# Kernel optimization log

Hardware: AMD Instinct MI355X
Metric: run time of the kernel (lower is better)

The kernel has to match this reference:

```python
import jax, jax.numpy as jnp
import numpy as np
import math

B, C, H, W = 2, 256, 64, 64
E = 256           # embed_dim
AE = 64           # angle embed dim = embed_dim // 4
NH = 3            # num angle hypotheses
HEADS = 8
HALF = AE // 2    # 32 sin/cos frequencies

# 3x3 kernel tap grid (dy, dx), row-major, matching torchvision DeformConv2d tap order
KY = jnp.array([-1,-1,-1, 0,0,0, 1,1,1], jnp.float32)
KX = jnp.array([-1, 0, 1,-1,0,1,-1,0,1], jnp.float32)
# assumed angle hypothesis deltas around the predicted angle
HYPO_DELTAS = (-math.pi/12, 0.0, math.pi/12)


def conv2d(x, w, b, pad):
    y = jax.lax.conv_general_dilated(x, w, (1, 1), [(pad, pad), (pad, pad)],
                                     dimension_numbers=('NCHW', 'OIHW', 'NCHW'))
    return y + b[None, :, None, None]


def gen_offsets(angles):
    """Rotate the base 3x3 kernel taps by the per-pixel angle; offset = rotated - base.
    angles: (B, H*W, 1) -> offsets (B, 18, H, W), (dy,dx) interleaved per tap."""
    a = angles.reshape(-1, H, W)
    c = jnp.cos(a)[..., None]           # (B,H,W,1)
    s = jnp.sin(a)[..., None]
    ry = KX * s + KY * c                # rotated y of each tap, (B,H,W,9)
    rx = KX * c - KY * s                # rotated x
    off = jnp.stack([ry - KY, rx - KX], axis=-1)   # (B,H,W,9,2)
    return off.reshape(-1, H, W, 18).transpose(0, 3, 1, 2)


def deform_conv(x, offsets, w, b):
    """DeformConv2d k=3, stride=1, pad=1, dilation=1, zero padding outside.
    x (B,C,H,W), offsets (B,18,H,W), w (O,C,3,3)."""
    off = offsets.reshape(x.shape[0], 9, 2, H, W)
    oy = off[:, :, 0].transpose(0, 2, 3, 1)          # (B,H,W,9)
    ox = off[:, :, 1].transpose(0, 2, 3, 1)
    hh = jnp.arange(H, dtype=jnp.float32)[None, :, None, None]
    ww = jnp.arange(W, dtype=jnp.float32)[None, None, :, None]
    py = hh + KY + oy                                # sample y, (B,H,W,9)
    px = ww + KX + ox
    y0 = jnp.floor(py)
    x0 = jnp.floor(px)
    wy = (py - y0)[:, None]                          # (B,1,H,W,9)
    wx = (px - x0)[:, None]

    def gather(yi, xi):
        valid = (yi >= 0) & (yi <= H - 1) & (xi >= 0) & (xi <= W - 1)
        yc = jnp.clip(yi, 0, H - 1).astype(jnp.int32)
        xc = jnp.clip(xi, 0, W - 1).astype(jnp.int32)
        g = jax.vmap(lambda img, yy, xx: img[:, yy, xx])(x, yc, xc)  # (B,C,H,W,9)
        return g * valid[:, None].astype(x.dtype)

    samp = (gather(y0, x0) * (1 - wy) * (1 - wx)
            + gather(y0, x0 + 1) * (1 - wy) * wx
            + gather(y0 + 1, x0) * wy * (1 - wx)
            + gather(y0 + 1, x0 + 1) * wy * wx)      # (B,C,H,W,9)
    w9 = w.reshape(w.shape[0], w.shape[1], 9)
    return jnp.einsum('bchwk,ock->bohw', samp, w9) + b[None, :, None, None]


def angle_encode(angles, freq_mult, w1, b1, ln_g, ln_b, w2, b2):
    an = (angles / (math.pi / 2))[..., 0]                       # (B,HW) le90 norm
    dim_t = jnp.arange(HALF, dtype=jnp.float32) / HALF * math.pi
    ae = an[..., None] * (freq_mult * dim_t)                    # (B,HW,HALF)
    emb = jnp.concatenate([jnp.sin(ae), jnp.cos(ae)], axis=-1)  # (B,HW,AE)
    h = emb @ w1.T + b1
    mu = h.mean(-1, keepdims=True)
    var = h.var(-1, keepdims=True)
    h = (h - mu) * jax.lax.rsqrt(var + 1e-5) * ln_g + ln_b
    return jax.nn.relu(h) @ w2.T + b2


def mha(q, kv, in_w, in_b, out_w, out_b):
    # q (L,1,E), kv (L,NH,E); torch nn.MultiheadAttention math
    wq, wk, wv = jnp.split(in_w, 3, axis=0)
    bq, bk, bv = jnp.split(in_b, 3)
    hd = E // HEADS
    Q = (q @ wq.T + bq).reshape(-1, 1, HEADS, hd).transpose(0, 2, 1, 3)
    K = (kv @ wk.T + bk).reshape(-1, NH, HEADS, hd).transpose(0, 2, 1, 3)
    V = (kv @ wv.T + bv).reshape(-1, NH, HEADS, hd).transpose(0, 2, 1, 3)
    attn = jax.nn.softmax(jnp.einsum('lhqd,lhkd->lhqk', Q, K) / math.sqrt(hd), axis=-1)
    o = jnp.einsum('lhqk,lhkd->lhqd', attn, V).transpose(0, 2, 1, 3).reshape(-1, 1, E)
    return o @ out_w.T + out_b


def group_norm(x, g, b, groups=32, eps=1e-5):
    Bq, Cc, Hh, Ww = x.shape
    xg = x.reshape(Bq, groups, Cc // groups, Hh, Ww)
    mu = xg.mean((2, 3, 4), keepdims=True)
    var = xg.var((2, 3, 4), keepdims=True)
    xn = ((xg - mu) * jax.lax.rsqrt(var + eps)).reshape(x.shape)
    return xn * g[None, :, None, None] + b[None, :, None, None]


def setup_inputs() -> dict:
    key = jax.random.key(0)
    ks = iter(jax.random.split(key, 32))
    r = lambda *s: jax.random.normal(next(ks), s, jnp.float32) * 0.05
    z = lambda *s: jnp.zeros(s, jnp.float32)
    return {
        'features': jax.random.normal(next(ks), (B, C, H, W), jnp.float32),
        'ap_w1': r(C // 4, C, 3, 3), 'ap_b1': z(C // 4),
        'ap_w2': r(1, C // 4, 1, 1), 'ap_b2': z(1),
        'freq_mult': jnp.ones((HALF,), jnp.float32),
        'ae_w1': r(AE, AE), 'ae_b1': z(AE),
        'ae_ln_g': jnp.ones((AE,), jnp.float32), 'ae_ln_b': z(AE),
        'ae_w2': r(AE, AE), 'ae_b2': z(AE),
        'dc_w': r(E, C, 3, 3), 'dc_b': z(E),
        'attn_in_w': r(3 * E, E), 'attn_in_b': z(3 * E),
        'attn_out_w': r(E, E), 'attn_out_b': z(E),
        'ja_w1': r(E, E + AE, 1, 1), 'ja_b1': z(E),
        'ja_w2': r(E, E, 1, 1), 'ja_b2': z(E),
        'op_w1': r(E, E, 3, 3), 'op_b1': z(E),
        'gn_g': jnp.ones((E,), jnp.float32), 'gn_b': z(E),
        'op_w2': r(E, E, 1, 1), 'op_b2': z(E),
    }


def reference(features, ap_w1, ap_b1, ap_w2, ap_b2, freq_mult, ae_w1, ae_b1,
              ae_ln_g, ae_ln_b, ae_w2, ae_b2, dc_w, dc_b, attn_in_w, attn_in_b,
              attn_out_w, attn_out_b, ja_w1, ja_b1, ja_w2, ja_b2, op_w1, op_b1,
              gn_g, gn_b, op_w2, op_b2):
    # 1) angle prediction
    h1 = jax.nn.relu(conv2d(features, ap_w1, ap_b1, 1))
    angles = conv2d(h1, ap_w2, ap_b2, 0).reshape(B, H * W, 1)
    # 2) periodic angle encoding
    angle_embed = angle_encode(angles, freq_mult, ae_w1, ae_b1, ae_ln_g, ae_ln_b, ae_w2, ae_b2)
    # 3) rotation-aware deformable alignment
    aligned = deform_conv(features, gen_offsets(angles), dc_w, dc_b)
    # 4) multi-angle hypotheses fused by per-pixel attention
    cand = [deform_conv(features, gen_offsets(angles + d), dc_w, dc_b) for d in HYPO_DELTAS]
    feat_stack = jnp.stack(cand, axis=1)                       # (B,NH,E,H,W)
    q = aligned.transpose(0, 2, 3, 1).reshape(B * H * W, 1, E)
    kv = feat_stack.transpose(0, 3, 4, 1, 2).reshape(B * H * W, NH, E)
    fused = mha(q, kv, attn_in_w, attn_in_b, attn_out_w, attn_out_b)
    fused = fused.reshape(B, H, W, E).transpose(0, 3, 1, 2)
    # 5) joint angle-spatial attention gate
    ae_sp = angle_embed.reshape(B, H, W, AE).transpose(0, 3, 1, 2)
    ji = jnp.concatenate([fused, ae_sp], axis=1)
    gate = jax.nn.sigmoid(conv2d(jax.nn.relu(conv2d(ji, ja_w1, ja_b1, 0)), ja_w2, ja_b2, 0))
    enh = fused * gate + fused
    # 6) output projection
    o = jax.nn.relu(group_norm(conv2d(enh, op_w1, op_b1, 1), gn_g, gn_b))
    return conv2d(o, op_w2, op_b2, 0)
```

## Files before the change

kernel.cpp:

```cpp
#include <hip/hip_runtime.h>

#define PI_F 3.14159265358979323846f
#define HWSZ 4096
#define NPIX 8192

typedef __attribute__((ext_vector_type(8))) short short8;
typedef __attribute__((ext_vector_type(4))) short short4_t;
typedef __attribute__((ext_vector_type(4))) float f32x4;

__device__ __forceinline__ short f2bf(float x){
  unsigned u = __float_as_uint(x);
  unsigned r = (u + 0x7FFFu + ((u >> 16) & 1u)) >> 16;
  return (short)r;
}
__device__ __forceinline__ float bf2f(short v){
  return __uint_as_float(((unsigned)(unsigned short)v) << 16);
}

__device__ __forceinline__ float wsum64(float v){
  #pragma unroll
  for (int m = 32; m >= 1; m >>= 1) v += __shfl_xor(v, m, 64);
  return v;
}
__device__ __forceinline__ float wsum8(float v){
  v += __shfl_xor(v, 1, 64);
  v += __shfl_xor(v, 2, 64);
  v += __shfl_xor(v, 4, 64);
  return v;
}

__device__ __forceinline__ void gl_lds(const short* g, short* s){
  __builtin_amdgcn_global_load_lds(
      (const __attribute__((address_space(1))) unsigned int*)g,
      (__attribute__((address_space(3))) unsigned int*)s, 16, 0, 0);
}

__global__ void k_prepall(const float* __restrict__ dc_w, const float* __restrict__ op_w1,
    const float* __restrict__ ap_w1, const float* __restrict__ features,
    const float* __restrict__ s0, const float* __restrict__ s1,
    const float* __restrict__ s2, const float* __restrict__ s3, const float* __restrict__ s4,
    short* __restrict__ enh_pad, short* __restrict__ Bdc, short* __restrict__ B2op,
    short* __restrict__ B3, short* __restrict__ feat_bf, short* __restrict__ A3,
    short* __restrict__ d0, short* __restrict__ d1,
    short* __restrict__ d2, short* __restrict__ d3, short* __restrict__ d4){
  __shared__ short tile[2304];
  __shared__ float ft[32][33];
  int bx = blockIdx.x, tid = threadIdx.x;
  if (bx < 2178){
    int i = bx*256 + tid;
    if (i < 557568) ((short4_t*)enh_pad)[i] = (short4_t){0,0,0,0};
  } else if (bx < 2434){
    int o = bx - 2178;
    const float* wo = dc_w + (size_t)o*2304;
    for (int i = tid; i < 2304; i += 256){
      int c = i / 9, k = i - c*9;
      tile[k*256 + c] = f2bf(wo[i]);
    }
    __syncthreads();
    for (int i = tid; i < 2304; i += 256){
      int k = i >> 8, c = i & 255;
      Bdc[((size_t)(k*256 + o))*256 + c] = tile[i];
    }
  } else if (bx < 2690){
    int o = bx - 2434;
    const float* wo = op_w1 + (size_t)o*2304;
    for (int i = tid; i < 2304; i += 256){
      int c = i / 9, k = i - c*9;
      tile[k*256 + c] = f2bf(wo[i]);
    }
    __syncthreads();
    short* out = B2op + (size_t)o*2304;
    for (int i = tid; i < 2304; i += 256) out[i] = tile[i];
  } else if (bx < 3330){
    int n = bx - 2690, c = tid;
    short hi = 0;
    if (n < 576){
      int o = n & 63, k = n >> 6;
      hi = f2bf(ap_w1[((size_t)o*256 + c)*9 + k]);
    }
    B3[(size_t)n*512 + c] = hi;
    B3[(size_t)n*512 + 256 + c] = hi;
  } else if (bx < 5186){
    int i = (bx - 3330)*256 + tid;
    if (i < 196608) d0[i] = f2bf(s0[i]);
    else if (i < 262144) d1[i-196608] = f2bf(s1[i-196608]);
    else if (i < 344064) d2[i-262144] = f2bf(s2[i-262144]);
    else if (i < 409600) d3[i-344064] = f2bf(s3[i-344064]);
    else if (i < 475136) d4[i-409600] = f2bf(s4[i-409600]);
  } else {
    int bid = bx - 5186;
    int z = bid >> 10;
    int rem = bid & 1023;
    int p0 = (rem & 127)*32, c0 = (rem >> 7)*32;
    int tx = tid & 31, ty = tid >> 5;
    #pragma unroll
    for (int i = ty; i < 32; i += 8)
      ft[i][tx] = features[((size_t)z*256 + c0 + i)*HWSZ + p0 + tx];
    __syncthreads();
    #pragma unroll
    for (int i = ty; i < 32; i += 8){
      float x = ft[tx][i];
      short hi = f2bf(x);
      short lo = f2bf(x - bf2f(hi));
      size_t p = (size_t)z*HWSZ + p0 + i;
      feat_bf[p*256 + c0 + tx] = hi;
      A3[p*512 + c0 + tx] = hi;
      A3[p*512 + 256 + c0 + tx] = lo;
    }
  }
}

template<int EPI, int BM, int BN = 128>
__global__ __launch_bounds__(256) void k_gemml(const short* __restrict__ A,
    const short* __restrict__ B, void* __restrict__ Cv,
    const float* __restrict__ bias, const short* __restrict__ aux,
    int K, int ldc){
  constexpr int NWC = BN/64;
  constexpr int NWR = 4/NWC;
  constexpr int WM = BM/NWR;
  constexpr int AF = WM/16;
  __shared__ alignas(16) short sA[2][BM*32];
  __shared__ alignas(16) short sB[2][BN*32];
  int tid = threadIdx.x;
  int w = tid >> 6, l = tid & 63;
  int wc = w % NWC, wr = w / NWC;
  int ml = l & 15, g = l >> 4;
  int srow = tid >> 2;
  int sch = (tid & 3)*8;
  int m0 = blockIdx.x*BM, n0 = blockIdx.y*BN;
  const short* Agp = A + (size_t)(m0 + srow)*K + sch;
  const short* Bgp = B + (size_t)(n0 + srow)*K + sch;
  short* sAd = &sA[0][srow*32 + sch];
  short* sBd = &sB[0][srow*32 + sch];
  f32x4 acc[AF][4];
  #pragma unroll
  for (int i = 0; i < AF; ++i)
    #pragma unroll
    for (int j = 0; j < 4; ++j) acc[i][j] = (f32x4){0.f,0.f,0.f,0.f};

  #define STAGE(bf, kt) { \
    _Pragma("unroll") \
    for (int c = 0; c < BM/64; ++c) \
      gl_lds(Agp + (size_t)(c*64)*K + (kt)*32, sAd + (bf)*BM*32 + c*2048); \
    _Pragma("unroll") \
    for (int c = 0; c < BN/64; ++c) \
      gl_lds(Bgp + (size_t)(c*64)*K + (kt)*32, sBd + (bf)*BN*32 + c*2048); \
  }
  int nk = K >> 5;
  STAGE(0, 0)
  int buf = 0;
  for (int kt = 0; kt < nk; ++kt){
    __syncthreads();
    if (kt + 1 < nk){ STAGE(buf^1, kt+1) }
    short8 af[AF], bq[4];
    #pragma unroll
    for (int i = 0; i < AF; ++i)
      af[i] = *(const short8*)&sA[buf][(wr*WM + i*16 + ml)*32 + g*8];
    #pragma unroll
    for (int j = 0; j < 4; ++j)
      bq[j] = *(const short8*)&sB[buf][(wc*64 + j*16 + ml)*32 + g*8];
    #pragma unroll
    for (int i = 0; i < AF; ++i)
      #pragma unroll
      for (int j = 0; j < 4; ++j)
        acc[i][j] = __builtin_amdgcn_mfma_f32_16x16x32_bf16(af[i], bq[j], acc[i][j], 0, 0, 0);
    buf ^= 1;
  }
  #undef STAGE

  int m0w = m0 + wr*WM;
  int n0w = n0 + wc*64;
  if constexpr (EPI == 4){
    __shared__ float cst[BM][129];
    #pragma unroll
    for (int fm = 0; fm < AF; ++fm)
      #pragma unroll
      for (int fn = 0; fn < 4; ++fn)
        #pragma unroll
        for (int r = 0; r < 4; ++r){
          int cl = wc*64 + fn*16 + ml;
          cst[wr*WM + fm*16 + g*4 + r][cl] = acc[fm][fn][r] + bias[blockIdx.y*128 + cl];
        }
    __syncthreads();
    int px0 = blockIdx.x*BM;
    int b = px0 >> 12, hw0 = px0 & 4095;
    int o = tid >> 1, seg = (tid & 1)*(BM/2);
    float* op = (float*)Cv + (((size_t)(b*256 + blockIdx.y*128 + o)) << 12) + hw0 + seg;
    #pragma unroll
    for (int i = 0; i < BM/2; i += 4){
      float4 vv = {cst[seg+i][o], cst[seg+i+1][o], cst[seg+i+2][o], cst[seg+i+3][o]};
      *(float4*)(op + i) = vv;
    }
  } else {
    #pragma unroll
    for (int fm = 0; fm < AF; ++fm)
      #pragma unroll
      for (int fn = 0; fn < 4; ++fn)
        #pragma unroll
        for (int r = 0; r < 4; ++r){
          int row = m0w + fm*16 + g*4 + r;
          int col = n0w + fn*16 + ml;
          float v = acc[fm][fn][r];
          if constexpr (EPI == 0){
            ((short*)Cv)[(size_t)row*ldc + col] = f2bf(v);
          } else if constexpr (EPI == 1){
            ((short*)Cv)[(size_t)row*ldc + col] = f2bf(v + bias[col]);
          } else if constexpr (EPI == 2){
            ((short*)Cv)[(size_t)row*ldc + col] = f2bf(fmaxf(v + bias[col], 0.f));
          } else if constexpr (EPI == 3){
            float f = bf2f(aux[(size_t)row*320 + col]);
            float s = 1.f/(1.f + __expf(-(v + bias[col])));
            ((short*)Cv)[(size_t)row*ldc + col] = f2bf(f * (1.f + s));
          } else if constexpr (EPI == 6){
            float f = bf2f(aux[(size_t)row*320 + col]);
            float s = 1.f/(1.f + __expf(-(v + bias[col])));
            int b = row >> 12, hw = row & 4095;
            int pi = b*4356 + ((hw>>6)+1)*66 + (hw&63) + 1;
            ((short*)Cv)[(size_t)pi*256 + col] = f2bf(f * (1.f + s));
          } else if constexpr (EPI == 7){
            ((short*)Cv)[(size_t)(col>>8)*2097152 + (size_t)row*256 + (col&255)] = f2bf(v);
          } else {
            ((float*)Cv)[(size_t)row*ldc + col] = v;
          }
        }
  }
}

__global__ __launch_bounds__(256) void k_qkv(const short* __restrict__ cand,
    const short* __restrict__ inw, const float* __restrict__ inb,
    short* __restrict__ KV, short* __restrict__ Qb){
  const short* A; const short* B; short* C; const float* bias; int ldc, m0, n0;
  if (blockIdx.y < 4){
    A = cand; B = inw + (size_t)256*256; C = KV; bias = inb + 256; ldc = 512;
    m0 = blockIdx.x*128; n0 = blockIdx.y*128;
  } else {
    if (blockIdx.x >= 128) return;
    A = cand + (size_t)NPIX*256; B = inw; C = Qb; bias = inb; ldc = 256;
    m0 = (blockIdx.x >> 1)*128; n0 = (blockIdx.x & 1)*128;
  }
  __shared__ alignas(16) short sA[2][128*32];
  __shared__ alignas(16) short sB[2][128*32];
  int tid = threadIdx.x;
  int w = tid >> 6, l = tid & 63;
  int wc = w & 1, wr = w >> 1;
  int ml = l & 15, g = l >> 4;
  int srow = tid >> 2;
  int sch = (tid & 3)*8;
  const short* Agp = A + (size_t)(m0 + srow)*256 + sch;
  const short* Bgp = B + (size_t)(n0 + srow)*256 + sch;
  short* sAd = &sA[0][srow*32 + sch];
  short* sBd = &sB[0][srow*32 + sch];
  f32x4 acc[4][4];
  #pragma unroll
  for (int i = 0; i < 4; ++i)
    #pragma unroll
    for (int j = 0; j < 4; ++j) acc[i][j] = (f32x4){0.f,0.f,0.f,0.f};
  #define STG2(bf, kt) { \
    gl_lds(Agp + (kt)*32, sAd + (bf)*4096); \
    gl_lds(Agp + (size_t)64*256 + (kt)*32, sAd + (bf)*4096 + 2048); \
    gl_lds(Bgp + (kt)*32, sBd + (bf)*4096); \
    gl_lds(Bgp + (size_t)64*256 + (kt)*32, sBd + (bf)*4096 + 2048); \
  }
  STG2(0, 0)
  int buf = 0;
  for (int kt = 0; kt < 8; ++kt){
    __syncthreads();
    if (kt + 1 < 8){ STG2(buf^1, kt+1) }
    short8 af[4], bq[4];
    #pragma unroll
    for (int i = 0; i < 4; ++i)
      af[i] = *(const short8*)&sA[buf][(wr*64 + i*16 + ml)*32 + g*8];
    #pragma unroll
    for (int j = 0; j < 4; ++j)
      bq[j] = *(const short8*)&sB[buf][(wc*64 + j*16 + ml)*32 + g*8];
    #pragma unroll
    for (int i = 0; i < 4; ++i)
      #pragma unroll
      for (int j = 0; j < 4; ++j)
        acc[i][j] = __builtin_amdgcn_mfma_f32_16x16x32_bf16(af[i], bq[j], acc[i][j], 0, 0, 0);
    buf ^= 1;
  }
  #undef STG2
  int m0w = m0 + wr*64;
  int n0w = n0 + wc*64;
  #pragma unroll
  for (int fm = 0; fm < 4; ++fm)
    #pragma unroll
    for (int fn = 0; fn < 4; ++fn)
      #pragma unroll
      for (int r = 0; r < 4; ++r){
        int row = m0w + fm*16 + g*4 + r;
        int col = n0w + fn*16 + ml;
        C[(size_t)row*ldc + col] = f2bf(acc[fm][fn][r] + bias[col]);
      }
}

__global__ __launch_bounds__(256) void k_attnproj(const short* __restrict__ Qb,
    const short* __restrict__ KVb, const short* __restrict__ wot,
    const float* __restrict__ outb, short* __restrict__ gateA){
  __shared__ alignas(16) short sO[64*256];
  __shared__ alignas(16) short sB[2][64*32];
  int tid = threadIdx.x;
  int m0 = blockIdx.x*64, n0 = blockIdx.y*64;
  int srow = tid >> 2, sch = (tid & 3)*8;
  const short* Bgp = wot + (size_t)(n0 + srow)*256 + sch;
  short* sBd = &sB[0][srow*32 + sch];
  gl_lds(Bgp, sBd);
  int lane = tid & 63;
  int sub = tid >> 6;
  const float sc = 0.17677669529663688f;
  #pragma unroll 2
  for (int it = 0; it < 16; ++it){
    int lp = it*4 + sub;
    int p = m0 + lp;
    float q[4];
    { short4_t t = *(const short4_t*)(Qb + (size_t)p*256 + lane*4);
      #pragma unroll
      for (int j = 0; j < 4; ++j) q[j] = bf2f(t[j]); }
    float kv[3][2][4];
    #pragma unroll
    for (int i = 0; i < 3; ++i){
      const short* rp = KVb + (size_t)(i*NPIX + p)*512 + lane*4;
      short4_t kt = *(const short4_t*)rp;
      short4_t vt = *(const short4_t*)(rp + 256);
      #pragma unroll
      for (int j = 0; j < 4; ++j){ kv[i][0][j] = bf2f(kt[j]); kv[i][1][j] = bf2f(vt[j]); }
    }
    float s[3];
    #pragma unroll
    for (int i = 0; i < 3; ++i){
      float d = 0.f;
      #pragma unroll
      for (int j = 0; j < 4; ++j) d = fmaf(q[j], kv[i][0][j], d);
      s[i] = wsum8(d) * sc;
    }
    float m = fmaxf(s[0], fmaxf(s[1], s[2]));
    float e0 = __expf(s[0]-m), e1 = __expf(s[1]-m), e2 = __expf(s[2]-m);
    float inv = 1.f/(e0+e1+e2);
    short4_t ot;
    #pragma unroll
    for (int j = 0; j < 4; ++j)
      ot[j] = f2bf((e0*kv[0][1][j] + e1*kv[1][1][j] + e2*kv[2][1][j]) * inv);
    *(short4_t*)&sO[lp*256 + lane*4] = ot;
  }
  int w = sub, ml = lane & 15, g = lane >> 4;
  f32x4 acc[4];
  #pragma unroll
  for (int j = 0; j < 4; ++j) acc[j] = (f32x4){0.f,0.f,0.f,0.f};
  int buf = 0;
  for (int kt = 0; kt < 8; ++kt){
    __syncthreads();
    if (kt + 1 < 8) gl_lds(Bgp + (kt+1)*32, sBd + (buf^1)*2048);
    short8 af = *(const short8*)&sO[(w*16 + ml)*256 + kt*32 + g*8];
    short8 bq[4];
    #pragma unroll
    for (int j = 0; j < 4; ++j)
      bq[j] = *(const short8*)&sB[buf][(j*16 + ml)*32 + g*8];
    #pragma unroll
    for (int j = 0; j < 4; ++j)
      acc[j] = __builtin_amdgcn_mfma_f32_16x16x32_bf16(af, bq[j], acc[j], 0, 0, 0);
    buf ^= 1;
  }
  int m0w = m0 + w*16;
  #pragma unroll
  for (int fn = 0; fn < 4; ++fn)
    #pragma unroll
    for (int r = 0; r < 4; ++r){
      int row = m0w + g*4 + r;
      int col = n0 + fn*16 + ml;
      gateA[(size_t)row*320 + col] = f2bf(acc[fn][r] + outb[col]);
    }
}

__global__ __launch_bounds__(256) void k_igconv(const short* __restrict__ Xpad,
    const short* __restrict__ B2, float* __restrict__ PG){
  __shared__ alignas(16) short sA[2][64*32];
  __shared__ alignas(16) short sB[2][128*32];
  int zg = blockIdx.z;
  int tid = threadIdx.x;
  int w = tid >> 6, l = tid & 63;
  int wr = w & 1, wc = w >> 1;
  int ml = l & 15, g = l >> 4;
  int srow = tid >> 2;
  int sch = (tid & 3)*8;
  int m0 = blockIdx.x*64, n0 = blockIdx.y*128;
  int b = blockIdx.x >> 6, imgrow = blockIdx.x & 63;
  int qbase = b*4356 + (imgrow+1)*66 + srow + 1;
  const short* Bgp = B2 + (size_t)(n0 + srow)*2304 + zg*768 + sch;
  short* sAd = &sA[0][srow*32 + sch];
  short* sBd = &sB[0][srow*32 + sch];
  int toff[3];
  #pragma unroll
  for (int i = 0; i < 3; ++i){
    int t = zg*3 + i;
    toff[i] = (t/3 - 1)*66 + (t%3) - 1;
  }
  f32x4 acc[2][4];
  #pragma unroll
  for (int i = 0; i < 2; ++i)
    #pragma unroll
    for (int j = 0; j < 4; ++j) acc[i][j] = (f32x4){0.f,0.f,0.f,0.f};

  #define STG(bf, kt) { \
    int tap = (kt) >> 3, cofs = ((kt) & 7)*32; \
    gl_lds(Xpad + (size_t)(qbase + toff[tap])*256 + cofs + sch, sAd + (bf)*2048); \
    gl_lds(Bgp + (kt)*32, sBd + (bf)*4096); \
    gl_lds(Bgp + (size_t)64*2304 + (kt)*32, sBd + (bf)*4096 + 2048); \
  }
  STG(0, 0)
  int buf = 0;
  for (int kt = 0; kt < 24; ++kt){
    __syncthreads();
    if (kt < 23){ STG(buf^1, kt+1) }
    short8 af[2], bq[4];
    #pragma unroll
    for (int i = 0; i < 2; ++i)
      af[i] = *(const short8*)&sA[buf][(wr*32 + i*16 + ml)*32 + g*8];
    #pragma unroll
    for (int j = 0; j < 4; ++j)
      bq[j] = *(const short8*)&sB[buf][(wc*64 + j*16 + ml)*32 + g*8];
    #pragma unroll
    for (int i = 0; i < 2; ++i)
      #pragma unroll
      for (int j = 0; j < 4; ++j)
        acc[i][j] = __builtin_amdgcn_mfma_f32_16x16x32_bf16(af[i], bq[j], acc[i][j], 0, 0, 0);
    buf ^= 1;
  }
  #undef STG

  float* out = PG + (size_t)zg*2097152;
  int m0w = m0 + wr*32;
  int n0w = n0 + wc*64;
  #pragma unroll
  for (int fm = 0; fm < 2; ++fm)
    #pragma unroll
    for (int fn = 0; fn < 4; ++fn)
      #pragma unroll
      for (int r = 0; r < 4; ++r){
        int row = m0w + fm*16 + g*4 + r;
        int col = n0w + fn*16 + ml;
        out[(size_t)row*256 + col] = acc[fm][fn][r];
      }
}

__global__ void k_aph1enc(const float* __restrict__ T, const float* __restrict__ b1,
    const float* __restrict__ w2, const float* __restrict__ b2,
    const float* __restrict__ freq,
    const float* __restrict__ ew1, const float* __restrict__ eb1,
    const float* __restrict__ lng, const float* __restrict__ lnb,
    const float* __restrict__ ew2, const float* __restrict__ eb2,
    short* __restrict__ gateA, int2* __restrict__ moff, float4* __restrict__ mw){
  const int KYi[9] = {-1,-1,-1,0,0,0,1,1,1};
  const int KXi[9] = {-1,0,1,-1,0,1,-1,0,1};
  __shared__ float sang[4];
  int lane = threadIdx.x & 63;
  int wid = threadIdx.x >> 6;
  int p = blockIdx.x*4 + wid;
  int hw = p & 4095;
  int h = hw >> 6, w = hw & 63;
  float acc = b1[lane];
  #pragma unroll
  for (int k = 0; k < 9; ++k){
    int y = h + KYi[k], x = w + KXi[k];
    if (y < 0 || y > 63 || x < 0 || x > 63) continue;
    acc += T[(size_t)(p + KYi[k]*64 + KXi[k])*640 + k*64 + lane];
  }
  float av = wsum64(fmaxf(acc, 0.f) * w2[lane]) + b2[0];
  if (lane == 0) sang[wid] = av;
  float an = av * (2.0f / PI_F);
  int f = lane & 31;
  float ph = an * freq[f] * ((float)f * (PI_F / 32.0f));
  float emb = (lane < 32) ? __sinf(ph) : __cosf(ph);
  float hh = eb1[lane];
  const float* w1r = ew1 + lane*64;
  #pragma unroll 8
  for (int i = 0; i < 64; ++i){
    float e = __shfl(emb, i, 64);
    hh = fmaf(e, w1r[i], hh);
  }
  float mu = wsum64(hh) * (1.0f/64.0f);
  float d = hh - mu;
  float var = wsum64(d*d) * (1.0f/64.0f);
  float hn = fmaf(d * rsqrtf(var + 1e-5f), lng[lane], lnb[lane]);
  float r = fmaxf(hn, 0.f);
  float o = eb2[lane];
  const float* w2r = ew2 + lane*64;
  #pragma unroll 8
  for (int i = 0; i < 64; ++i){
    float e = __shfl(r, i, 64);
    o = fmaf(e, w2r[i], o);
  }
  gateA[(size_t)p*320 + 256 + lane] = f2bf(o);
  __syncthreads();
  int tid = threadIdx.x;
  if (tid < 108){
    int lp = tid / 27;
    int j = tid - lp*27;
    int pp = blockIdx.x*4 + lp;
    int hyp = j / 9;
    int tap = j - hyp*9;
    float ky = (float)(tap/3 - 1), kx = (float)(tap - (tap/3)*3 - 1);
    float a = sang[lp] + ((float)hyp - 1.0f) * (PI_F / 12.0f);
    float sn = __sinf(a), cs = __cosf(a);
    int b2i = pp >> 12, hw2 = pp & 4095;
    float py = (float)(hw2 >> 6) + kx*sn + ky*cs;
    float px = (float)(hw2 & 63) + kx*cs - ky*sn;
    float y0f = floorf(py), x0f = floorf(px);
    float wy = py - y0f, wx = px - x0f;
    int y0 = (int)y0f, x0 = (int)x0f;
    bool vx0 = (unsigned)x0 < 64u, vx1 = (unsigned)(x0+1) < 64u;
    bool vy0 = (unsigned)y0 < 64u, vy1 = (unsigned)(y0+1) < 64u;
    int xb = vx0 ? x0 : (vx1 ? x0+1 : 0);
    float sx0 = vx0 ? 1.f-wx : (vx1 ? wx : 0.f);
    float sx1 = (vx0 && vx1) ? wx : 0.f;
    int ry0 = vy0 ? y0 : 0;
    int ry1 = vy1 ? y0+1 : 0;
    float vw0 = vy0 ? 1.f-wy : 0.f;
    float vw1 = vy1 ? wy : 0.f;
    int base = (b2i << 12);
    int mi = pp*27 + j;
    moff[mi] = make_int2(tap*4194304 + (base + ry0*64 + xb)*512,
                         tap*4194304 + (base + ry1*64 + xb)*512);
    mw[mi] = make_float4(vw0*sx0, vw0*sx1, vw1*sx0, vw1*sx1);
  }
}

__global__ __launch_bounds__(256, 4) void k_sample(const short* __restrict__ G,
    const int2* __restrict__ moff, const float4* __restrict__ mw,
    const float* __restrict__ bias, short* __restrict__ cand){
  __shared__ int2 smo[216];
  __shared__ float4 smw[216];
  int id = blockIdx.x;
  int sw = (id & 7)*128 + (id >> 3);
  int tid = threadIdx.x;
  int pbase = sw*8;
  if (tid < 216){
    smo[tid] = moff[pbase*27 + tid];
    smw[tid] = mw[pbase*27 + tid];
  }
  __syncthreads();
  int lp = (tid >> 6)*2 + ((tid >> 5) & 1);
  int p = pbase + lp;
  int c8 = (tid & 31)*8;
  float av[3][8];
  {
    float4 b0 = *(const float4*)(bias + c8);
    float4 b1 = *(const float4*)(bias + c8 + 4);
    #pragma unroll
    for (int h2 = 0; h2 < 3; ++h2){
      av[h2][0]=b0.x; av[h2][1]=b0.y; av[h2][2]=b0.z; av[h2][3]=b0.w;
      av[h2][4]=b1.x; av[h2][5]=b1.y; av[h2][6]=b1.z; av[h2][7]=b1.w;
    }
  }
  #pragma unroll
  for (int hyp = 0; hyp < 3; ++hyp){
    #pragma unroll 3
    for (int tap = 0; tap < 9; ++tap){
      int idx = lp*27 + hyp*9 + tap;
      int2 o = smo[idx];
      float4 wv = smw[idx];
      const short* r0 = (const short*)((const char*)G + o.x) + c8;
      const short* r1 = (const short*)((const char*)G + o.y) + c8;
      short8 v00 = *(const short8*)r0;
      short8 v01 = *(const short8*)(r0 + 256);
      short8 v10 = *(const short8*)r1;
      short8 v11 = *(const short8*)(r1 + 256);
      #pragma unroll
      for (int e = 0; e < 8; ++e){
        float s = wv.x*bf2f(v00[e]) + wv.y*bf2f(v01[e]);
        s += wv.z*bf2f(v10[e]) + wv.w*bf2f(v11[e]);
        av[hyp][e] += s;
      }
    }
  }
  #pragma unroll
  for (int hyp = 0; hyp < 3; ++hyp){
    short8 o;
    #pragma unroll
    for (int e = 0; e < 8; ++e) o[e] = f2bf(av[hyp][e]);
    *(short8*)(cand + ((size_t)hyp*NPIX + p)*256 + c8) = o;
  }
}

__global__ void k_sum3stat(const float* __restrict__ PG, const float* __restrict__ bias,
    float* __restrict__ t, float* __restrict__ spart){
  int p0 = blockIdx.x * 8;
  int c = threadIdx.x;
  float bb = bias[c];
  float s = 0.f, s2 = 0.f;
  #pragma unroll
  for (int pp = 0; pp < 8; ++pp){
    size_t idx = (size_t)(p0+pp)*256 + c;
    float v = PG[idx] + PG[idx + 2097152] + PG[idx + 4194304] + bb;
    t[idx] = v;
    s += v; s2 = fmaf(v, v, s2);
  }
  s  += __shfl_xor(s, 1, 64);  s  += __shfl_xor(s, 2, 64);  s  += __shfl_xor(s, 4, 64);
  s2 += __shfl_xor(s2, 1, 64); s2 += __shfl_xor(s2, 2, 64); s2 += __shfl_xor(s2, 4, 64);
  if ((c & 7) == 0){
    int b = p0 >> 12;
    int bg = b*32 + (c >> 3);
    int blk = blockIdx.x & 511;
    spart[(size_t)(bg*512 + blk)*2]     = s;
    spart[(size_t)(bg*512 + blk)*2 + 1] = s2;
  }
}

__global__ void k_gnfin(const float* __restrict__ spart, float* __restrict__ stat){
  int bg = blockIdx.x;
  const float* sp = spart + (size_t)bg*1024;
  float s = 0.f, s2 = 0.f;
  for (int i = threadIdx.x; i < 512; i += 256){
    s += sp[i*2]; s2 += sp[i*2+1];
  }
  s = wsum64(s); s2 = wsum64(s2);
  __shared__ float rs[4], rs2[4];
  int wid = threadIdx.x >> 6;
  if ((threadIdx.x & 63) == 0){ rs[wid] = s; rs2[wid] = s2; }
  __syncthreads();
  if (threadIdx.x == 0){
    float S = rs[0]+rs[1]+rs[2]+rs[3];
    float S2 = rs2[0]+rs2[1]+rs2[2]+rs2[3];
    float mean = S * (1.f/32768.f);
    float var = S2 * (1.f/32768.f) - mean*mean;
    stat[bg*2]   = mean;
    stat[bg*2+1] = rsqrtf(var + 1e-5f);
  }
}

__global__ __launch_bounds__(256) void k_gnproj(const float* __restrict__ t,
    const float* __restrict__ stat, const float* __restrict__ gng,
    const float* __restrict__ gnb, const short* __restrict__ w2,
    const float* __restrict__ b2, float* __restrict__ out){
  __shared__ float cst[64*132];
  __shared__ alignas(16) short sB[2][128*32];
  short* sA = (short*)cst;
  int tid = threadIdx.x;
  int m0 = blockIdx.x*64;
  int b = m0 >> 12;
  int srow = tid >> 2, sch = (tid & 3)*8;
  const short* Bgp = w2 + (size_t)(blockIdx.y*128 + srow)*256 + sch;
  short* sBd = &sB[0][srow*32 + sch];
  gl_lds(Bgp, sBd);
  gl_lds(Bgp + (size_t)64*256, sBd + 2048);
  #pragma unroll 4
  for (int it = 0; it < 16; ++it){
    int c = it*256 + tid;
    int row = c >> 6;
    int col = (c & 63)*4;
    int g4 = col >> 3;
    float mean = stat[(b*32+g4)*2], rstd = stat[(b*32+g4)*2+1];
    float4 v = *(const float4*)(t + (size_t)(m0+row)*256 + col);
    float4 gg = *(const float4*)(gng + col);
    float4 bbv = *(const float4*)(gnb + col);
    short4_t o;
    o[0] = f2bf(fmaxf((v.x - mean)*rstd*gg.x + bbv.x, 0.f));
    o[1] = f2bf(fmaxf((v.y - mean)*rstd*gg.y + bbv.y, 0.f));
    o[2] = f2bf(fmaxf((v.z - mean)*rstd*gg.z + bbv.z, 0.f));
    o[3] = f2bf(fmaxf((v.w - mean)*rstd*gg.w + bbv.w, 0.f));
    *(short4_t*)&sA[row*256 + col] = o;
  }
  int w = tid >> 6, l = tid & 63;
  int wr = w & 1, wc = w >> 1;
  int ml = l & 15, g = l >> 4;
  f32x4 acc[2][4];
  #pragma unroll
  for (int i = 0; i < 2; ++i)
    #pragma unroll
    for (int j = 0; j < 4; ++j) acc[i][j] = (f32x4){0.f,0.f,0.f,0.f};
  int buf = 0;
  for (int kt = 0; kt < 8; ++kt){
    __syncthreads();
    if (kt + 1 < 8){
      gl_lds(Bgp + (kt+1)*32, sBd + (buf^1)*4096);
      gl_lds(Bgp + (size_t)64*256 + (kt+1)*32, sBd + (buf^1)*4096 + 2048);
    }
    short8 af[2], bq[4];
    #pragma unroll
    for (int i = 0; i < 2; ++i)
      af[i] = *(const short8*)&sA[(wr*32 + i*16 + ml)*256 + kt*32 + g*8];
    #pragma unroll
    for (int j = 0; j < 4; ++j)
      bq[j] = *(const short8*)&sB[buf][(wc*64 + j*16 + ml)*32 + g*8];
    #pragma unroll
    for (int i = 0; i < 2; ++i)
      #pragma unroll
      for (int j = 0; j < 4; ++j)
        acc[i][j] = __builtin_amdgcn_mfma_f32_16x16x32_bf16(af[i], bq[j], acc[i][j], 0, 0, 0);
    buf ^= 1;
  }
  __syncthreads();
  #pragma unroll
  for (int fm = 0; fm < 2; ++fm)
    #pragma unroll
    for (int fn = 0; fn < 4; ++fn)
      #pragma unroll
      for (int r = 0; r < 4; ++r){
        int cl = wc*64 + fn*16 + ml;
        cst[(wr*32 + fm*16 + g*4 + r)*132 + cl] = acc[fm][fn][r] + b2[blockIdx.y*128 + cl];
      }
  __syncthreads();
  int hw0 = m0 & 4095;
  int o = tid >> 1, seg = (tid & 1)*32;
  float* op = out + (((size_t)(b*256 + blockIdx.y*128 + o)) << 12) + hw0 + seg;
  #pragma unroll
  for (int i = 0; i < 32; i += 4){
    float4 vv = {cst[(seg+i)*132+o], cst[(seg+i+1)*132+o],
                 cst[(seg+i+2)*132+o], cst[(seg+i+3)*132+o]};
    *(float4*)(op + i) = vv;
  }
}

extern "C" void kernel_launch(void* const* d_in, const int* in_sizes, int n_in,
                              void* d_out, int out_size, void* d_ws, size_t ws_size,
                              hipStream_t stream){
  (void)in_sizes; (void)n_in; (void)out_size; (void)ws_size;
  const float* features   = (const float*)d_in[0];
  const float* ap_w1      = (const float*)d_in[1];
  const float* ap_b1      = (const float*)d_in[2];
  const float* ap_w2      = (const float*)d_in[3];
  const float* ap_b2      = (const float*)d_in[4];
  const float* freq       = (const float*)d_in[5];
  const float* ae_w1      = (const float*)d_in[6];
  const float* ae_b1      = (const float*)d_in[7];
  const float* ae_ln_g    = (const float*)d_in[8];
  const float* ae_ln_b    = (const float*)d_in[9];
  const float* ae_w2      = (const float*)d_in[10];
  const float* ae_b2      = (const float*)d_in[11];
  const float* dc_w       = (const float*)d_in[12];
  const float* dc_b       = (const float*)d_in[13];
  const float* attn_in_w  = (const float*)d_in[14];
  const float* attn_in_b  = (const float*)d_in[15];
  const float* attn_out_w = (const float*)d_in[16];
  const float* attn_out_b = (const float*)d_in[17];
  const float* ja_w1      = (const float*)d_in[18];
  const float* ja_b1      = (const float*)d_in[19];
  const float* ja_w2      = (const float*)d_in[20];
  const float* ja_b2      = (const float*)d_in[21];
  const float* op_w1      = (const float*)d_in[22];
  const float* op_b1      = (const float*)d_in[23];
  const float* gn_g       = (const float*)d_in[24];
  const float* gn_b       = (const float*)d_in[25];
  const float* op_w2      = (const float*)d_in[26];
  const float* op_b2      = (const float*)d_in[27];

  char* base = (char*)d_ws;
  #define ALLOC(ty, name, elems) ty* name = (ty*)base; base += (size_t)(elems)*sizeof(ty);
  ALLOC(short, feat_bf, 8192*256)
  ALLOC(short, Bdc,     2304*256)
  ALLOC(short, B2op,    256*2304)
  ALLOC(short, B3ap,    640*512)
  ALLOC(short, inw_bf,  768*256)
  ALLOC(short, wot_bf,  256*256)
  ALLOC(short, jw1_bf,  256*320)
  ALLOC(short, jw2_bf,  256*256)
  ALLOC(short, wop2_bf, 256*256)
  ALLOC(short, Gbuf,    24576*768)
  ALLOC(short, gguard,  64)
  ALLOC(short, cand_bf, 3*8192*256)
  ALLOC(short, gateA,   8192*320)
  ALLOC(short, hid_bf,  8192*256)
  ALLOC(short, enh_pad, 2*4356*256)
  ALLOC(float, tbuf,    8192*256)
  ALLOC(float, gstat,   128)
  ALLOC(float, spart,   65536)
  ALLOC(int,   moffb,   2*NPIX*27)
  ALLOC(float, mwb,     4*NPIX*27)
  #undef ALLOC
  (void)gguard;
  short* A3 = cand_bf;
  float* T_ap = (float*)Gbuf;
  short* KVbuf = Gbuf;
  short* Qbuf  = Gbuf + (size_t)24576*512;
  float* PG    = (float*)Gbuf;
  int2*  moff  = (int2*)moffb;
  float4* mwv  = (float4*)mwb;

  k_prepall<<<7234, 256, 0, stream>>>(dc_w, op_w1, ap_w1, features,
      attn_in_w, attn_out_w, ja_w1, ja_w2, op_w2,
      enh_pad, Bdc, B2op, B3ap, feat_bf, A3,
      inw_bf, wot_bf, jw1_bf, jw2_bf, wop2_bf);

  k_gemml<5,64><<<dim3(128,5), 256, 0, stream>>>(A3, B3ap, T_ap, nullptr, nullptr, 512, 640);
  k_aph1enc<<<2048, 256, 0, stream>>>(T_ap, ap_b1, ap_w2, ap_b2, freq,
                                      ae_w1, ae_b1, ae_ln_g, ae_ln_b, ae_w2, ae_b2,
                                      gateA, moff, mwv);
  k_gemml<7,128><<<dim3(64,18), 256, 0, stream>>>(feat_bf, Bdc, Gbuf, nullptr, nullptr, 256, 2304);
  k_sample<<<1024, 256, 0, stream>>>(Gbuf, moff, mwv, dc_b, cand_bf);
  k_qkv<<<dim3(192,5), 256, 0, stream>>>(cand_bf, inw_bf, attn_in_b, KVbuf, Qbuf);
  k_attnproj<<<dim3(128,4), 256, 0, stream>>>(Qbuf, KVbuf, wot_bf, attn_out_b, gateA);
  k_gemml<2,64,64><<<dim3(128,4), 256, 0, stream>>>(gateA, jw1_bf, hid_bf, ja_b1, nullptr, 320, 256);
  k_gemml<6,64,64><<<dim3(128,4), 256, 0, stream>>>(hid_bf, jw2_bf, enh_pad, ja_b2, gateA, 256, 256);
  k_igconv<<<dim3(128,2,3), 256, 0, stream>>>(enh_pad, B2op, PG);
  k_sum3stat<<<1024, 256, 0, stream>>>(PG, op_b1, tbuf, spart);
  k_gnfin<<<64, 256, 0, stream>>>(spart, gstat);
  k_gnproj<<<dim3(128,2), 256, 0, stream>>>(tbuf, gstat, gn_g, gn_b, wop2_bf, op_b2,
                                            (float*)d_out);
}
```

Measured before the change: 193.5 us.

## Merge angle-predictor GEMM and deform-conv tap GEMM into one launch

Combines the angle-predictor GEMM (A3 x B3, K=512) and the deform-conv tap GEMM (features x Bdc, K=256) into a single kernel whose grid y index chooses which GEMM a block computes. The deform GEMM now reads the hi half of A3 with stride 512, so the separate feat_bf copy and its writes in the prep kernel are removed. A3 and T_ap get their own workspace buffers instead of aliasing cand_bf and Gbuf, which the fused launch needs. This saves one launch and fills the GPU better, at the cost of more workspace memory and uneven per-block work (K=256 versus K=512 blocks).

```diff
diff --git a/kernel.cpp b/kernel.cpp
--- a/kernel.cpp
+++ b/kernel.cpp
@@ -40,7 +40,7 @@
     const float* __restrict__ s0, const float* __restrict__ s1,
     const float* __restrict__ s2, const float* __restrict__ s3, const float* __restrict__ s4,
     short* __restrict__ enh_pad, short* __restrict__ Bdc, short* __restrict__ B2op,
-    short* __restrict__ B3, short* __restrict__ feat_bf, short* __restrict__ A3,
+    short* __restrict__ B3, short* __restrict__ A3,
     short* __restrict__ d0, short* __restrict__ d1,
     short* __restrict__ d2, short* __restrict__ d3, short* __restrict__ d4){
   __shared__ short tile[2304];
@@ -103,11 +103,80 @@
       short hi = f2bf(x);
       short lo = f2bf(x - bf2f(hi));
       size_t p = (size_t)z*HWSZ + p0 + i;
-      feat_bf[p*256 + c0 + tx] = hi;
       A3[p*512 + c0 + tx] = hi;
       A3[p*512 + 256 + c0 + tx] = lo;
     }
   }
+}
+
+__global__ __launch_bounds__(256) void k_mainA(const short* __restrict__ A3,
+    const short* __restrict__ Bdc, const short* __restrict__ B3,
+    short* __restrict__ G, float* __restrict__ T){
+  __shared__ alignas(16) short sA[2][128*32];
+  __shared__ alignas(16) short sB[2][128*32];
+  bool isG = blockIdx.y < 18;
+  const short* B; int K, ldb, n0;
+  if (isG){ B = Bdc; K = 256; ldb = 256; n0 = blockIdx.y*128; }
+  else    { B = B3;  K = 512; ldb = 512; n0 = ((int)blockIdx.y - 18)*128; }
+  int tid = threadIdx.x;
+  int w = tid >> 6, l = tid & 63;
+  int wc = w & 1, wr = w >> 1;
+  int ml = l & 15, g = l >> 4;
+  int srow = tid >> 2;
+  int sch = (tid & 3)*8;
+  int m0 = blockIdx.x*128;
+  const short* Agp = A3 + (size_t)(m0 + srow)*512 + sch;
+  const short* Bgp = B + (size_t)(n0 + srow)*ldb + sch;
+  short* sAd = &sA[0][srow*32 + sch];
+  short* sBd = &sB[0][srow*32 + sch];
+  f32x4 acc[4][4];
+  #pragma unroll
+  for (int i = 0; i < 4; ++i)
+    #pragma unroll
+    for (int j = 0; j < 4; ++j) acc[i][j] = (f32x4){0.f,0.f,0.f,0.f};
+  #define STG(bf, kt) { \
+    gl_lds(Agp + (kt)*32, sAd + (bf)*4096); \
+    gl_lds(Agp + (size_t)64*512 + (kt)*32, sAd + (bf)*4096 + 2048); \
+    gl_lds(Bgp + (kt)*32, sBd + (bf)*4096); \
+    gl_lds(Bgp + (size_t)64*ldb + (kt)*32, sBd + (bf)*4096 + 2048); \
+  }
+  int nk = K >> 5;
+  STG(0, 0)
+  int buf = 0;
+  for (int kt = 0; kt < nk; ++kt){
+    __syncthreads();
+    if (kt + 1 < nk){ STG(buf^1, kt+1) }
+    short8 af[4], bq[4];
+    #pragma unroll
+    for (int i = 0; i < 4; ++i)
+      af[i] = *(const short8*)&sA[buf][(wr*64 + i*16 + ml)*32 + g*8];
+    #pragma unroll
+    for (int j = 0; j < 4; ++j)
+      bq[j] = *(const short8*)&sB[buf][(wc*64 + j*16 + ml)*32 + g*8];
+    #pragma unroll
+    for (int i = 0; i < 4; ++i)
+      #pragma unroll
+      for (int j = 0; j < 4; ++j)
+        acc[i][j] = __builtin_amdgcn_mfma_f32_16x16x32_bf16(af[i], bq[j], acc[i][j], 0, 0, 0);
+    buf ^= 1;
+  }
+  #undef STG
+  int m0w = m0 + wr*64;
+  int n0w = n0 + wc*64;
+  #pragma unroll
+  for (int fm = 0; fm < 4; ++fm)
+    #pragma unroll
+    for (int fn = 0; fn < 4; ++fn)
+      #pragma unroll
+      for (int r = 0; r < 4; ++r){
+        int row = m0w + fm*16 + g*4 + r;
+        int col = n0w + fn*16 + ml;
+        float v = acc[fm][fn][r];
+        if (isG)
+          G[(size_t)(col>>8)*2097152 + (size_t)row*256 + (col&255)] = f2bf(v);
+        else
+          T[(size_t)row*640 + col] = v;
+      }
 }
 
 template<int EPI, int BM, int BN = 128>
@@ -170,60 +239,25 @@
 
   int m0w = m0 + wr*WM;
   int n0w = n0 + wc*64;
-  if constexpr (EPI == 4){
-    __shared__ float cst[BM][129];
-    #pragma unroll
-    for (int fm = 0; fm < AF; ++fm)
-      #pragma unroll
-      for (int fn = 0; fn < 4; ++fn)
-        #pragma unroll
-        for (int r = 0; r < 4; ++r){
-          int cl = wc*64 + fn*16 + ml;
-          cst[wr*WM + fm*16 + g*4 + r][cl] = acc[fm][fn][r] + bias[blockIdx.y*128 + cl];
+  #pragma unroll
+  for (int fm = 0; fm < AF; ++fm)
+    #pragma unroll
+    for (int fn = 0; fn < 4; ++fn)
+      #pragma unroll
+      for (int r = 0; r < 4; ++r){
+        int row = m0w + fm*16 + g*4 + r;
+        int col = n0w + fn*16 + ml;
+        float v = acc[fm][fn][r];
+        if constexpr (EPI == 2){
+          ((short*)Cv)[(size_t)row*ldc + col] = f2bf(fmaxf(v + bias[col], 0.f));
+        } else if constexpr (EPI == 6){
+          float f = bf2f(aux[(size_t)row*320 + col]);
+          float s = 1.f/(1.f + __expf(-(v + bias[col])));
+          int b = row >> 12, hw = row & 4095;
+          int pi = b*4356 + ((hw>>6)+1)*66 + (hw&63) + 1;
+          ((short*)Cv)[(size_t)pi*256 + col] = f2bf(f * (1.f + s));
         }
-    __syncthreads();
-    int px0 = blockIdx.x*BM;
-    int b = px0 >> 12, hw0 = px0 & 4095;
-    int o = tid >> 1, seg = (tid & 1)*(BM/2);
-    float* op = (float*)Cv + (((size_t)(b*256 + blockIdx.y*128 + o)) << 12) + hw0 + seg;
-    #pragma unroll
-    for (int i = 0; i < BM/2; i += 4){
-      float4 vv = {cst[seg+i][o], cst[seg+i+1][o], cst[seg+i+2][o], cst[seg+i+3][o]};
-      *(float4*)(op + i) = vv;
-    }
-  } else {
-    #pragma unroll
-    for (int fm = 0; fm < AF; ++fm)
-      #pragma unroll
-      for (int fn = 0; fn < 4; ++fn)
-        #pragma unroll
-        for (int r = 0; r < 4; ++r){
-          int row = m0w + fm*16 + g*4 + r;
-          int col = n0w + fn*16 + ml;
-          float v = acc[fm][fn][r];
-          if constexpr (EPI == 0){
-            ((short*)Cv)[(size_t)row*ldc + col] = f2bf(v);
-          } else if constexpr (EPI == 1){
-            ((short*)Cv)[(size_t)row*ldc + col] = f2bf(v + bias[col]);
-          } else if constexpr (EPI == 2){
-            ((short*)Cv)[(size_t)row*ldc + col] = f2bf(fmaxf(v + bias[col], 0.f));
-          } else if constexpr (EPI == 3){
-            float f = bf2f(aux[(size_t)row*320 + col]);
-            float s = 1.f/(1.f + __expf(-(v + bias[col])));
-            ((short*)Cv)[(size_t)row*ldc + col] = f2bf(f * (1.f + s));
-          } else if constexpr (EPI == 6){
-            float f = bf2f(aux[(size_t)row*320 + col]);
-            float s = 1.f/(1.f + __expf(-(v + bias[col])));
-            int b = row >> 12, hw = row & 4095;
-            int pi = b*4356 + ((hw>>6)+1)*66 + (hw&63) + 1;
-            ((short*)Cv)[(size_t)pi*256 + col] = f2bf(f * (1.f + s));
-          } else if constexpr (EPI == 7){
-            ((short*)Cv)[(size_t)(col>>8)*2097152 + (size_t)row*256 + (col&255)] = f2bf(v);
-          } else {
-            ((float*)Cv)[(size_t)row*ldc + col] = v;
-          }
-        }
-  }
+      }
 }
 
 __global__ __launch_bounds__(256) void k_qkv(const short* __restrict__ cand,
@@ -746,7 +780,6 @@
 
   char* base = (char*)d_ws;
   #define ALLOC(ty, name, elems) ty* name = (ty*)base; base += (size_t)(elems)*sizeof(ty);
-  ALLOC(short, feat_bf, 8192*256)
   ALLOC(short, Bdc,     2304*256)
   ALLOC(short, B2op,    256*2304)
   ALLOC(short, B3ap,    640*512)
@@ -755,8 +788,10 @@
   ALLOC(short, jw1_bf,  256*320)
   ALLOC(short, jw2_bf,  256*256)
   ALLOC(short, wop2_bf, 256*256)
+  ALLOC(short, A3,      8192*512)
   ALLOC(short, Gbuf,    24576*768)
   ALLOC(short, gguard,  64)
+  ALLOC(float, T_ap,    8192*640)
   ALLOC(short, cand_bf, 3*8192*256)
   ALLOC(short, gateA,   8192*320)
   ALLOC(short, hid_bf,  8192*256)
@@ -768,8 +803,6 @@
   ALLOC(float, mwb,     4*NPIX*27)
   #undef ALLOC
   (void)gguard;
-  short* A3 = cand_bf;
-  float* T_ap = (float*)Gbuf;
   short* KVbuf = Gbuf;
   short* Qbuf  = Gbuf + (size_t)24576*512;
   float* PG    = (float*)Gbuf;
@@ -778,14 +811,13 @@
 
   k_prepall<<<7234, 256, 0, stream>>>(dc_w, op_w1, ap_w1, features,
       attn_in_w, attn_out_w, ja_w1, ja_w2, op_w2,
-      enh_pad, Bdc, B2op, B3ap, feat_bf, A3,
+      enh_pad, Bdc, B2op, B3ap, A3,
       inw_bf, wot_bf, jw1_bf, jw2_bf, wop2_bf);
 
-  k_gemml<5,64><<<dim3(128,5), 256, 0, stream>>>(A3, B3ap, T_ap, nullptr, nullptr, 512, 640);
+  k_mainA<<<dim3(64,23), 256, 0, stream>>>(A3, Bdc, B3ap, Gbuf, T_ap);
   k_aph1enc<<<2048, 256, 0, stream>>>(T_ap, ap_b1, ap_w2, ap_b2, freq,
                                       ae_w1, ae_b1, ae_ln_g, ae_ln_b, ae_w2, ae_b2,
                                       gateA, moff, mwv);
-  k_gemml<7,128><<<dim3(64,18), 256, 0, stream>>>(feat_bf, Bdc, Gbuf, nullptr, nullptr, 256, 2304);
   k_sample<<<1024, 256, 0, stream>>>(Gbuf, moff, mwv, dc_b, cand_bf);
   k_qkv<<<dim3(192,5), 256, 0, stream>>>(cand_bf, inw_bf, attn_in_b, KVbuf, Qbuf);
   k_attnproj<<<dim3(128,4), 256, 0, stream>>>(Qbuf, KVbuf, wot_bf, attn_out_b, gateA);
```

Measured after the change: 186.1 us. 1.04x faster.
